# Kernel tuning notes

Hardware: AMD Instinct MI355X
Metric: run time of the kernel (lower is better)

Reference implementation:

```python
import jax, jax.numpy as jnp
import numpy as np

NB_BINS = 10
N = 33554432  # 2**25 elements


def setup_inputs() -> dict:
    key = jax.random.key(0)
    k1, k2 = jax.random.split(key)
    logits = jax.random.normal(k1, (N,), dtype=jnp.float32)
    labels = jax.random.randint(k2, (N,), 0, 2, dtype=jnp.int32)
    return {"logits": logits, "labels": labels}


def reference(logits, labels):
    # confidences in (0,1); bins are (l, u] over linspace(0,1,nb+1),
    # so bin index = ceil(conf * nb) - 1, clipped to [0, nb-1].
    conf = jax.nn.sigmoid(logits)
    idx = jnp.clip(jnp.ceil(conf * NB_BINS).astype(jnp.int32) - 1, 0, NB_BINS - 1)

    counts = jax.ops.segment_sum(jnp.ones_like(conf), idx, num_segments=NB_BINS)
    sum_conf = jax.ops.segment_sum(conf, idx, num_segments=NB_BINS)
    sum_pos = jax.ops.segment_sum(labels.astype(conf.dtype), idx, num_segments=NB_BINS)

    denom = jnp.maximum(counts, 1.0)
    nonempty = counts > 0
    positives_per_bin = jnp.where(nonempty, sum_pos / denom, 0.0)
    confidence_per_bin = jnp.where(nonempty, sum_conf / denom, 0.0)
    return jnp.stack([positives_per_bin, confidence_per_bin])  # [2, nb_bins]
```

## Files before the change

kernel.cpp:

```cpp
#include <hip/hip_runtime.h>

typedef unsigned int u32;
typedef unsigned long long u64;

#define NB 10
#define BLOCKS 2048
#define TPB 256
#define ITERS 16
#define CHUNK_F4 64
#define WAVE_F4 (ITERS * CHUNK_F4)

typedef __attribute__((address_space(3))) char lds_char;
typedef __attribute__((address_space(1))) const char g_char;

__device__ __forceinline__ void dma16(const void* g, void* l) {
    __builtin_amdgcn_global_load_lds((g_char*)g, (lds_char*)l, 16, 0, 0);
}

#define WAIT_VM(nn)  __builtin_amdgcn_s_waitcnt(((nn) & 15) | 0xF70)
#define WAIT_LGKM0() __builtin_amdgcn_s_waitcnt(0xC07F)

#if defined(__has_builtin)
#if __has_builtin(__builtin_amdgcn_sched_barrier)
#define SCHEDB() __builtin_amdgcn_sched_barrier(0)
#else
#define SCHEDB()
#endif
#else
#define SCHEDB()
#endif

__global__ void rd_zero_ws(u32* __restrict__ ws) {
    if (threadIdx.x < 320) ws[threadIdx.x] = 0u;
}

__device__ __forceinline__ void rd_acc(float x, int lab,
                                       u64& c64, u64& p64, u64& flo, u64& fhi) {
    float e = __expf(-x);
    float conf = __builtin_amdgcn_rcpf(1.0f + e);
    float t10 = __builtin_fmaf(conf, 10.0f, -1e-6f);
    int b = min(9, (int)t10);
    float frac = t10 - (float)b;
    u32 ffx = (u32)__builtin_fmaf(frac, 127.0f, 0.5f);

    u32 sh6 = (u32)(b * 6);
    c64 += 1ull << sh6;
    p64 += ((u64)(u32)lab) << sh6;

    bool lo = b < 5;
    u32 sh12 = (u32)(b * 12);
    u32 shf = lo ? sh12 : (sh12 - 60u);
    u64 v = ((u64)ffx) << shf;
    flo += lo ? v : 0ull;
    fhi += lo ? 0ull : v;
}

__device__ __forceinline__ void rd_acc4(const float4& x, const int4& y,
                                        u64& c64, u64& p64, u64& flo, u64& fhi) {
    rd_acc(x.x, y.x, c64, p64, flo, fhi);
    rd_acc(x.y, y.y, c64, p64, flo, fhi);
    rd_acc(x.z, y.z, c64, p64, flo, fhi);
    rd_acc(x.w, y.w, c64, p64, flo, fhi);
}

__global__ __launch_bounds__(TPB) void rd_hist(const float* __restrict__ logits,
                                               const int* __restrict__ labels,
                                               u32* __restrict__ ws,
                                               long long n) {
    __shared__ __align__(16) char lds[16 * 1024];

    u32 cp[NB], cf[NB];
    #pragma unroll
    for (int b = 0; b < NB; ++b) { cp[b] = 0u; cf[b] = 0u; }

    const float4* l4 = (const float4*)logits;
    const int4*   i4 = (const int4*)labels;
    int lane = threadIdx.x & 63;
    int wave = threadIdx.x >> 6;
    long long nf4 = n >> 2;
    long long seg = (long long)blockIdx.x * (4 * WAVE_F4);

    if (seg + 4 * WAVE_F4 <= nf4) {
        long long gb = seg + (long long)wave * WAVE_F4;
        const float4* gl = l4 + gb + lane;
        const int4*   gi = i4 + gb + lane;
        char* myl = lds + wave * 4096;

        #define ISSUE(t, bb) do {                               \
            char* _base = myl + (bb) * 2048;                    \
            dma16(gl + (t) * CHUNK_F4, _base);                  \
            dma16(gi + (t) * CHUNK_F4, _base + 1024);           \
        } while (0)

        ISSUE(0, 0);
        ISSUE(1, 1);

        u64 c64 = 0, p64 = 0, flo = 0, fhi = 0;
        #pragma unroll
        for (int t = 0; t < ITERS; ++t) {
            const int bb = t & 1;
            const char* base = myl + bb * 2048;
            if (t < ITERS - 1) { WAIT_VM(2); } else { WAIT_VM(0); }
            SCHEDB();
            float4 xa = *(const float4*)(base + lane * 16);
            int4   ya = *(const int4*)(base + 1024 + lane * 16);
            WAIT_LGKM0();
            SCHEDB();
            if (t + 2 < ITERS) ISSUE(t + 2, bb);
            SCHEDB();
            rd_acc4(xa, ya, c64, p64, flo, fhi);
            if ((t & 7) == 7) {
                #pragma unroll
                for (int b = 0; b < NB; ++b) {
                    u32 cnt = (u32)(c64 >> (6 * b)) & 63u;
                    u32 pos = (u32)(p64 >> (6 * b)) & 63u;
                    cp[b] += cnt | (pos << 16);
                    cf[b] += (b < 5) ? ((u32)(flo >> (12 * b)) & 4095u)
                                     : ((u32)(fhi >> (12 * (b - 5))) & 4095u);
                }
                c64 = 0; p64 = 0; flo = 0; fhi = 0;
            }
        }
        #undef ISSUE
    }

    long long done_f4 = ((long long)gridDim.x < nf4 / (4 * WAVE_F4)
                             ? (long long)gridDim.x
                             : nf4 / (4 * WAVE_F4)) * (4 * WAVE_F4);
    long long tail = done_f4 * 4;
    if (tail < n) {
        long long tid    = (long long)blockIdx.x * blockDim.x + threadIdx.x;
        long long stride = (long long)gridDim.x * blockDim.x;
        for (long long i = tail + tid; i < n; i += stride) {
            float e = __expf(-logits[i]);
            float conf = __builtin_amdgcn_rcpf(1.0f + e);
            float t10 = __builtin_fmaf(conf, 10.0f, -1e-6f);
            int b = min(9, (int)t10);
            float frac = t10 - (float)b;
            u32 ffx = (u32)__builtin_fmaf(frac, 127.0f, 0.5f);
            atomicAdd((u64*)&ws[32 * b], (u64)ffx);
            atomicAdd(&ws[32 * b + 2], 1u);
            atomicAdd(&ws[32 * b + 3], (u32)labels[i]);
        }
    }

    __shared__ u32 s_cp[4][NB];
    __shared__ u32 s_cf[4][NB];
    #pragma unroll
    for (int b = 0; b < NB; ++b) {
        u32 c = cp[b];
        u32 f = cf[b];
        #pragma unroll
        for (int off = 32; off; off >>= 1) {
            c += __shfl_down(c, off, 64);
            f += __shfl_down(f, off, 64);
        }
        if (lane == 0) { s_cp[wave][b] = c; s_cf[wave][b] = f; }
    }
    __syncthreads();

    if (threadIdx.x < NB) {
        int b = threadIdx.x;
        u32 c = s_cp[0][b] + s_cp[1][b] + s_cp[2][b] + s_cp[3][b];
        u64 f = (u64)s_cf[0][b] + s_cf[1][b] + s_cf[2][b] + s_cf[3][b];
        atomicAdd((u64*)&ws[32 * b], f);
        atomicAdd(&ws[32 * b + 2], c & 0xFFFFu);
        atomicAdd(&ws[32 * b + 3], c >> 16);
    }
}

__global__ void rd_finalize(const u32* __restrict__ ws, float* __restrict__ out) {
    int b = threadIdx.x;
    if (b < NB) {
        u64 f   = *(const u64*)&ws[32 * b];
        u32 cnt = ws[32 * b + 2];
        u32 pos = ws[32 * b + 3];
        double sumconf = ((double)b * (double)cnt + (double)f * (1.0 / 127.0)) * 0.1;
        float denom = fmaxf((float)cnt, 1.0f);
        bool ne = cnt > 0u;
        out[b]      = ne ? ((float)pos / denom) : 0.0f;
        out[NB + b] = ne ? (float)(sumconf / (double)denom) : 0.0f;
    }
}

extern "C" void kernel_launch(void* const* d_in, const int* in_sizes, int n_in,
                              void* d_out, int out_size, void* d_ws, size_t ws_size,
                              hipStream_t stream) {
    const float* logits = (const float*)d_in[0];
    const int*   labels = (const int*)d_in[1];
    float* out = (float*)d_out;
    u32*   ws  = (u32*)d_ws;
    long long n = (long long)in_sizes[0];

    rd_zero_ws<<<1, 512, 0, stream>>>(ws);
    rd_hist<<<BLOCKS, TPB, 0, stream>>>(logits, labels, ws, n);
    rd_finalize<<<1, 64, 0, stream>>>(ws, out);
}
```

Before: 306.0 us.

## Replace LDS DMA double-buffering with register prefetch ring, halve grid

Removes the global_load_lds path with manual waitcnt and scheduling barriers. Each lane now keeps a 4-deep register ring of float4/int4 prefetches straight from global memory. The grid drops to 1024 blocks with 32 iterations each, and launch bounds request 4 blocks per CU. This is meant to cut LDS round trips and wait overhead and to keep more loads in flight per wave. The cost is higher register pressure and leaving the scheduling of loads to the compiler.

```diff
diff --git a/kernel.cpp b/kernel.cpp
--- a/kernel.cpp
+++ b/kernel.cpp
@@ -4,31 +4,11 @@
 typedef unsigned long long u64;
 
 #define NB 10
-#define BLOCKS 2048
+#define BLOCKS 1024
 #define TPB 256
-#define ITERS 16
-#define CHUNK_F4 64
-#define WAVE_F4 (ITERS * CHUNK_F4)
-
-typedef __attribute__((address_space(3))) char lds_char;
-typedef __attribute__((address_space(1))) const char g_char;
-
-__device__ __forceinline__ void dma16(const void* g, void* l) {
-    __builtin_amdgcn_global_load_lds((g_char*)g, (lds_char*)l, 16, 0, 0);
-}
-
-#define WAIT_VM(nn)  __builtin_amdgcn_s_waitcnt(((nn) & 15) | 0xF70)
-#define WAIT_LGKM0() __builtin_amdgcn_s_waitcnt(0xC07F)
-
-#if defined(__has_builtin)
-#if __has_builtin(__builtin_amdgcn_sched_barrier)
-#define SCHEDB() __builtin_amdgcn_sched_barrier(0)
-#else
-#define SCHEDB()
-#endif
-#else
-#define SCHEDB()
-#endif
+#define ITERS 32
+#define DEPTH 4
+#define WAVE_F4 (ITERS * 64)
 
 __global__ void rd_zero_ws(u32* __restrict__ ws) {
     if (threadIdx.x < 320) ws[threadIdx.x] = 0u;
@@ -63,12 +43,10 @@
     rd_acc(x.w, y.w, c64, p64, flo, fhi);
 }
 
-__global__ __launch_bounds__(TPB) void rd_hist(const float* __restrict__ logits,
-                                               const int* __restrict__ labels,
-                                               u32* __restrict__ ws,
-                                               long long n) {
-    __shared__ __align__(16) char lds[16 * 1024];
-
+__global__ __launch_bounds__(TPB, 4) void rd_hist(const float* __restrict__ logits,
+                                                  const int* __restrict__ labels,
+                                                  u32* __restrict__ ws,
+                                                  long long n) {
     u32 cp[NB], cf[NB];
     #pragma unroll
     for (int b = 0; b < NB; ++b) { cp[b] = 0u; cf[b] = 0u; }
@@ -80,48 +58,45 @@
     long long nf4 = n >> 2;
     long long seg = (long long)blockIdx.x * (4 * WAVE_F4);
 
+    u64 c64 = 0, p64 = 0, flo = 0, fhi = 0;
+
+    #define UNPACK() do {                                                   \
+        _Pragma("unroll")                                                   \
+        for (int b = 0; b < NB; ++b) {                                      \
+            u32 cnt = (u32)(c64 >> (6 * b)) & 63u;                          \
+            u32 pos = (u32)(p64 >> (6 * b)) & 63u;                          \
+            cp[b] += cnt | (pos << 16);                                     \
+            cf[b] += (b < 5) ? ((u32)(flo >> (12 * b)) & 4095u)             \
+                             : ((u32)(fhi >> (12 * (b - 5))) & 4095u);      \
+        }                                                                   \
+        c64 = 0; p64 = 0; flo = 0; fhi = 0;                                 \
+    } while (0)
+
     if (seg + 4 * WAVE_F4 <= nf4) {
         long long gb = seg + (long long)wave * WAVE_F4;
         const float4* gl = l4 + gb + lane;
         const int4*   gi = i4 + gb + lane;
-        char* myl = lds + wave * 4096;
 
-        #define ISSUE(t, bb) do {                               \
-            char* _base = myl + (bb) * 2048;                    \
-            dma16(gl + (t) * CHUNK_F4, _base);                  \
-            dma16(gi + (t) * CHUNK_F4, _base + 1024);           \
-        } while (0)
+        float4 px0 = gl[0 * 64], px1 = gl[1 * 64], px2 = gl[2 * 64], px3 = gl[3 * 64];
+        int4   py0 = gi[0 * 64], py1 = gi[1 * 64], py2 = gi[2 * 64], py3 = gi[3 * 64];
 
-        ISSUE(0, 0);
-        ISSUE(1, 1);
-
-        u64 c64 = 0, p64 = 0, flo = 0, fhi = 0;
         #pragma unroll
         for (int t = 0; t < ITERS; ++t) {
-            const int bb = t & 1;
-            const char* base = myl + bb * 2048;
-            if (t < ITERS - 1) { WAIT_VM(2); } else { WAIT_VM(0); }
-            SCHEDB();
-            float4 xa = *(const float4*)(base + lane * 16);
-            int4   ya = *(const int4*)(base + 1024 + lane * 16);
-            WAIT_LGKM0();
-            SCHEDB();
-            if (t + 2 < ITERS) ISSUE(t + 2, bb);
-            SCHEDB();
-            rd_acc4(xa, ya, c64, p64, flo, fhi);
-            if ((t & 7) == 7) {
-                #pragma unroll
-                for (int b = 0; b < NB; ++b) {
-                    u32 cnt = (u32)(c64 >> (6 * b)) & 63u;
-                    u32 pos = (u32)(p64 >> (6 * b)) & 63u;
-                    cp[b] += cnt | (pos << 16);
-                    cf[b] += (b < 5) ? ((u32)(flo >> (12 * b)) & 4095u)
-                                     : ((u32)(fhi >> (12 * (b - 5))) & 4095u);
-                }
-                c64 = 0; p64 = 0; flo = 0; fhi = 0;
+            const int s = t & 3;
+            float4 x; int4 y;
+            if      (s == 0) { x = px0; y = py0; }
+            else if (s == 1) { x = px1; y = py1; }
+            else if (s == 2) { x = px2; y = py2; }
+            else             { x = px3; y = py3; }
+            if (t + DEPTH < ITERS) {
+                if      (s == 0) { px0 = gl[(t + DEPTH) * 64]; py0 = gi[(t + DEPTH) * 64]; }
+                else if (s == 1) { px1 = gl[(t + DEPTH) * 64]; py1 = gi[(t + DEPTH) * 64]; }
+                else if (s == 2) { px2 = gl[(t + DEPTH) * 64]; py2 = gi[(t + DEPTH) * 64]; }
+                else             { px3 = gl[(t + DEPTH) * 64]; py3 = gi[(t + DEPTH) * 64]; }
             }
+            rd_acc4(x, y, c64, p64, flo, fhi);
+            if ((t & 7) == 7) UNPACK();
         }
-        #undef ISSUE
     }
 
     long long done_f4 = ((long long)gridDim.x < nf4 / (4 * WAVE_F4)
@@ -143,6 +118,7 @@
             atomicAdd(&ws[32 * b + 3], (u32)labels[i]);
         }
     }
+    #undef UNPACK
 
     __shared__ u32 s_cp[4][NB];
     __shared__ u32 s_cf[4][NB];
```

New measurement: 296.1 us. 3.2% less time.
